# Kernel tuning notes

Hardware: AMD Instinct MI355X
Metric: run time of the kernel (lower is better)

The kernel has to match this reference:

```python
import jax, jax.numpy as jnp
import numpy as np

B, S, H, NH = 8, 1024, 768, 12
DK = H // NH  # 64


def setup_inputs() -> dict:
    key = jax.random.key(0)
    ks = jax.random.split(key, 7)
    sc = 0.02
    return {
        "Q": jax.random.normal(ks[0], (B, S, H), jnp.float32),
        "K": jax.random.normal(ks[1], (B, S, H), jnp.float32),
        "V": jax.random.normal(ks[2], (B, S, H), jnp.float32),
        "Wq": jax.random.normal(ks[3], (H, H), jnp.float32) * sc,
        "Wk": jax.random.normal(ks[4], (H, H), jnp.float32) * sc,
        "Wv": jax.random.normal(ks[5], (H, H), jnp.float32) * sc,
        "Wo": jax.random.normal(ks[6], (H, H), jnp.float32) * sc,
    }


def reference(Q, K, V, Wq, Wk, Wv, Wo):
    # torch Linear(bias=False): y = x @ W.T, weight shape [out, in]
    q = jnp.einsum('bsh,oh->bso', Q, Wq).reshape(B, S, NH, DK)
    k = jnp.einsum('bsh,oh->bso', K, Wk).reshape(B, S, NH, DK)
    v = jnp.einsum('bsh,oh->bso', V, Wv).reshape(B, S, NH, DK)
    # naive SDPA per head: full [B,NH,S,S] score matrix, scale by sqrt(dk)
    scores = jnp.einsum('bqnd,bknd->bnqk', q, k) / jnp.sqrt(jnp.float32(DK))
    w = jax.nn.softmax(scores, axis=-1)
    c = jnp.einsum('bnqk,bknd->bqnd', w, v).reshape(B, S, H)
    return jnp.einsum('bsh,oh->bso', c, Wo)
```

## Files before the change

kernel.cpp:

```cpp
#include <hip/hip_runtime.h>
#include <hip/hip_bf16.h>

#define B_   8
#define S_   1024
#define H_   768
#define NH_  12
#define DK_  64
#define M_   (B_ * S_)

typedef __attribute__((ext_vector_type(8))) short          short8;
typedef __attribute__((ext_vector_type(8))) unsigned short ushort8;
typedef __attribute__((ext_vector_type(4))) unsigned short ushort4v;
typedef __attribute__((ext_vector_type(4))) float          f32x4;

__device__ __forceinline__ unsigned short f2bf(float x) {
    union { __hip_bfloat16 h; unsigned short u; } r;
    r.h = __float2bfloat16(x);
    return r.u;
}

__device__ __forceinline__ unsigned cvtpk_bf16(float lo, float hi) {
    unsigned r;
    asm("v_cvt_pk_bf16_f32 %0, %1, %2" : "=v"(r) : "v"(lo), "v"(hi));
    return r;
}

__global__ __launch_bounds__(256)
void cvt_w(const float* __restrict__ w0, const float* __restrict__ w1,
           const float* __restrict__ w2, const float* __restrict__ w3,
           unsigned short* __restrict__ o0, unsigned short* __restrict__ o1,
           unsigned short* __restrict__ o2, unsigned short* __restrict__ o3)
{
    const int wsel = blockIdx.y;
    const float* src = (wsel == 0) ? w0 : (wsel == 1) ? w1 : (wsel == 2) ? w2 : w3;
    unsigned short* dst = (wsel == 0) ? o0 : (wsel == 1) ? o1 : (wsel == 2) ? o2 : o3;
    const float s = (wsel == 0) ? 0.125f * 1.44269504089f : 1.0f;
    const int i = blockIdx.x * 256 + threadIdx.x;
    const float4 x = ((const float4*)src)[i];
    ushort4v o;
    o[0] = f2bf(x.x * s); o[1] = f2bf(x.y * s);
    o[2] = f2bf(x.z * s); o[3] = f2bf(x.w * s);
    ((ushort4v*)dst)[i] = o;
}

template<bool A_BF16, bool OUT_BF16>
__global__ __launch_bounds__(256)
void gemm_bt(const void* __restrict__ A0, const void* __restrict__ A1,
             const void* __restrict__ A2,
             const unsigned short* __restrict__ W0,
             const unsigned short* __restrict__ W1,
             const unsigned short* __restrict__ W2,
             void* __restrict__ C0, void* __restrict__ C1, void* __restrict__ C2)
{
    __shared__ unsigned short As[128 * 32];
    __shared__ unsigned short Bs[128 * 32];

    const int tid  = threadIdx.x;
    const int z    = blockIdx.z;
    const int bm   = blockIdx.x, bn = blockIdx.y;
    const int w    = tid >> 6, lane = tid & 63;
    const int lg   = lane >> 4, lc = lane & 15;
    const int wm   = (w >> 1) * 64, wn = (w & 1) * 64;

    const void* Av = (z == 0) ? A0 : (z == 1) ? A1 : A2;
    const unsigned short* Bw = (z == 0) ? W0 : (z == 1) ? W1 : W2;
    void* Cv = (z == 0) ? C0 : (z == 1) ? C1 : C2;

    const float*          Af = (const float*)Av;
    const unsigned short* Ah = (const unsigned short*)Av;

    f32x4 acc[4][4] = {};

    for (int k0 = 0; k0 < H_; k0 += 32) {
        if (A_BF16) {
#pragma unroll
            for (int i = 0; i < 2; i++) {
                const int gI = i * 256 + tid;
                const int row = gI >> 2, c8 = (gI & 3) * 8;
                *(ushort8*)&As[row * 32 + c8] =
                    *(const ushort8*)&Ah[(size_t)(bm * 128 + row) * H_ + k0 + c8];
            }
        } else {
#pragma unroll
            for (int i = 0; i < 4; i++) {
                const int gI = i * 256 + tid;
                const int row = gI >> 3, c4 = (gI & 7) * 4;
                const float4 x = *(const float4*)&Af[(size_t)(bm * 128 + row) * H_ + k0 + c4];
                ushort4v o4;
                o4[0] = f2bf(x.x); o4[1] = f2bf(x.y);
                o4[2] = f2bf(x.z); o4[3] = f2bf(x.w);
                *(ushort4v*)&As[row * 32 + c4] = o4;
            }
        }
#pragma unroll
        for (int i = 0; i < 2; i++) {
            const int gI = i * 256 + tid;
            const int row = gI >> 2, c8 = (gI & 3) * 8;
            *(ushort8*)&Bs[row * 32 + c8] =
                *(const ushort8*)&Bw[(size_t)(bn * 128 + row) * H_ + k0 + c8];
        }
        __syncthreads();

        short8 af[4], bfr[4];
#pragma unroll
        for (int mi = 0; mi < 4; mi++)
            af[mi] = *(const short8*)&As[(wm + mi * 16 + lc) * 32 + lg * 8];
#pragma unroll
        for (int ni = 0; ni < 4; ni++)
            bfr[ni] = *(const short8*)&Bs[(wn + ni * 16 + lc) * 32 + lg * 8];
#pragma unroll
        for (int mi = 0; mi < 4; mi++)
#pragma unroll
            for (int ni = 0; ni < 4; ni++)
                acc[mi][ni] = __builtin_amdgcn_mfma_f32_16x16x32_bf16(
                    af[mi], bfr[ni], acc[mi][ni], 0, 0, 0);
        __syncthreads();
    }

#pragma unroll
    for (int mi = 0; mi < 4; mi++)
#pragma unroll
        for (int ni = 0; ni < 4; ni++)
#pragma unroll
            for (int reg = 0; reg < 4; reg++) {
                const int row = bm * 128 + wm + mi * 16 + lg * 4 + reg;
                const int col = bn * 128 + wn + ni * 16 + lc;
                if (OUT_BF16)
                    ((unsigned short*)Cv)[(size_t)row * H_ + col] = f2bf(acc[mi][ni][reg]);
                else
                    ((float*)Cv)[(size_t)row * H_ + col] = acc[mi][ni][reg];
            }
}

__global__ __launch_bounds__(256)
void attn(const unsigned short* __restrict__ q,
          const unsigned short* __restrict__ k,
          const unsigned short* __restrict__ v,
          unsigned short* __restrict__ c)
{
    __shared__ unsigned short Ks[64][72];
    __shared__ unsigned short Vt[64][72];

    const int tid  = threadIdx.x;
    const int qt   = blockIdx.x, h = blockIdx.y, b = blockIdx.z;
    const int wid  = tid >> 6;
    const int lane = tid & 63;
    const int lg   = lane >> 4, lc = lane & 15;
    const int r    = tid >> 2;
    const int d0   = (tid & 3) * 16;
    const int g    = tid & 3;
    const size_t base = (size_t)b * S_ * H_ + (size_t)h * DK_;

    short8 aq[2][2];
#pragma unroll
    for (int m = 0; m < 2; m++)
#pragma unroll
        for (int ks = 0; ks < 2; ks++)
            aq[m][ks] = *(const short8*)
                &q[base + (size_t)(qt * 128 + wid * 32 + m * 16 + lc) * H_ + ks * 32 + lg * 8];

    f32x4 o[2][4] = {};
    float mrow[2] = {-1e30f, -1e30f}, lrow[2] = {0.f, 0.f};

    for (int kt = 0; kt < S_ / 64; kt++) {
        {
            const unsigned short* ksrc = &k[base + (size_t)(kt * 64 + r) * H_ + d0];
            *(ushort8*)&Ks[r][d0]     = *(const ushort8*)ksrc;
            *(ushort8*)&Ks[r][d0 + 8] = *(const ushort8*)(ksrc + 8);
            const unsigned short* vsrc = &v[base + (size_t)(kt * 64 + r) * H_ + d0];
            const ushort8 v0 = *(const ushort8*)vsrc;
            const ushort8 v1 = *(const ushort8*)(vsrc + 8);
            const int colv = r ^ (g << 4);
#pragma unroll
            for (int j = 0; j < 8; j++) Vt[d0 + j][colv]     = v0[j];
#pragma unroll
            for (int j = 0; j < 8; j++) Vt[d0 + 8 + j][colv] = v1[j];
        }
        __syncthreads();

        f32x4 st[2][4] = {};
#pragma unroll
        for (int ni = 0; ni < 4; ni++)
#pragma unroll
            for (int ks = 0; ks < 2; ks++) {
                const short8 bk = *(const short8*)&Ks[ni * 16 + lc][ks * 32 + lg * 8];
                st[0][ni] = __builtin_amdgcn_mfma_f32_16x16x32_bf16(bk, aq[0][ks], st[0][ni], 0, 0, 0);
                st[1][ni] = __builtin_amdgcn_mfma_f32_16x16x32_bf16(bk, aq[1][ks], st[1][ni], 0, 0, 0);
            }

        unsigned pw[2][4][2];
#pragma unroll
        for (int m = 0; m < 2; m++) {
            float pm = st[m][0][0];
#pragma unroll
            for (int ni = 0; ni < 4; ni++)
#pragma unroll
                for (int reg = 0; reg < 4; reg++)
                    pm = fmaxf(pm, st[m][ni][reg]);
            pm = fmaxf(pm, __shfl_xor(pm, 16, 64));
            pm = fmaxf(pm, __shfl_xor(pm, 32, 64));
            const float mnew  = fmaxf(mrow[m], pm);
            const float scale = exp2f(mrow[m] - mnew);
            float psum = 0.f;
#pragma unroll
            for (int ni = 0; ni < 4; ni++)
#pragma unroll
                for (int reg = 0; reg < 4; reg++) {
                    const float p = exp2f(st[m][ni][reg] - mnew);
                    st[m][ni][reg] = p; psum += p;
                }
            psum += __shfl_xor(psum, 16, 64);
            psum += __shfl_xor(psum, 32, 64);
            lrow[m] = lrow[m] * scale + psum;
            mrow[m] = mnew;

            float scr[4];
#pragma unroll
            for (int reg = 0; reg < 4; reg++)
                scr[reg] = __shfl(scale, lg * 4 + reg, 64);
#pragma unroll
            for (int ni = 0; ni < 4; ni++)
#pragma unroll
                for (int reg = 0; reg < 4; reg++)
                    o[m][ni][reg] *= scr[reg];

#pragma unroll
            for (int ni = 0; ni < 4; ni++) {
                pw[m][ni][0] = cvtpk_bf16(st[m][ni][0], st[m][ni][1]);
                pw[m][ni][1] = cvtpk_bf16(st[m][ni][2], st[m][ni][3]);
            }
        }

        const int sl0 = lc + ((lg & 1) << 5);
        const int sl1 = sl0 + 16;
        const bool hi = (lg >> 1) != 0;
        short8 pa[2][2];
#pragma unroll
        for (int m = 0; m < 2; m++)
#pragma unroll
            for (int ks = 0; ks < 2; ks++) {
                const unsigned lo0 = pw[m][2 * ks][0],     lo1 = pw[m][2 * ks][1];
                const unsigned hi0 = pw[m][2 * ks + 1][0], hi1 = pw[m][2 * ks + 1][1];
                union { unsigned u[4]; short8 s8; } pk;
                const unsigned a0l = __shfl(lo0, sl0, 64), a0h = __shfl(hi0, sl0, 64);
                const unsigned a1l = __shfl(lo1, sl0, 64), a1h = __shfl(hi1, sl0, 64);
                const unsigned a2l = __shfl(lo0, sl1, 64), a2h = __shfl(hi0, sl1, 64);
                const unsigned a3l = __shfl(lo1, sl1, 64), a3h = __shfl(hi1, sl1, 64);
                pk.u[0] = hi ? a0h : a0l;
                pk.u[1] = hi ? a1h : a1l;
                pk.u[2] = hi ? a2h : a2l;
                pk.u[3] = hi ? a3h : a3l;
                pa[m][ks] = pk.s8;
            }

#pragma unroll
        for (int ni = 0; ni < 4; ni++)
#pragma unroll
            for (int ks = 0; ks < 2; ks++) {
                const short8 bv = *(const short8*)
                    &Vt[ni * 16 + lc][(ks * 32 + lg * 8) ^ (ni << 4)];
                o[0][ni] = __builtin_amdgcn_mfma_f32_16x16x32_bf16(pa[0][ks], bv, o[0][ni], 0, 0, 0);
                o[1][ni] = __builtin_amdgcn_mfma_f32_16x16x32_bf16(pa[1][ks], bv, o[1][ni], 0, 0, 0);
            }
        __syncthreads();
    }

#pragma unroll
    for (int m = 0; m < 2; m++) {
        const float iv = 1.0f / lrow[m];
#pragma unroll
        for (int reg = 0; reg < 4; reg++) {
            const float ivr = __shfl(iv, lg * 4 + reg, 64);
            const int row = qt * 128 + wid * 32 + m * 16 + lg * 4 + reg;
#pragma unroll
            for (int ni = 0; ni < 4; ni++)
                c[base + (size_t)row * H_ + ni * 16 + lc] = f2bf(o[m][ni][reg] * ivr);
        }
    }
}

extern "C" void kernel_launch(void* const* d_in, const int* in_sizes, int n_in,
                              void* d_out, int out_size, void* d_ws, size_t ws_size,
                              hipStream_t stream)
{
    const float* Q  = (const float*)d_in[0];
    const float* K  = (const float*)d_in[1];
    const float* V  = (const float*)d_in[2];
    const float* Wq = (const float*)d_in[3];
    const float* Wk = (const float*)d_in[4];
    const float* Wv = (const float*)d_in[5];
    const float* Wo = (const float*)d_in[6];

    unsigned short* qb = (unsigned short*)d_ws;
    unsigned short* kb = qb + (size_t)M_ * H_;
    unsigned short* vb = kb + (size_t)M_ * H_;
    unsigned short* cb = vb + (size_t)M_ * H_;
    unsigned short* wq = cb + (size_t)M_ * H_;
    unsigned short* wk = wq + (size_t)H_ * H_;
    unsigned short* wv = wk + (size_t)H_ * H_;
    unsigned short* wo = wv + (size_t)H_ * H_;

    cvt_w<<<dim3(H_ * H_ / 4 / 256, 4), 256, 0, stream>>>(
        Wq, Wk, Wv, Wo, wq, wk, wv, wo);

    gemm_bt<false, true><<<dim3(M_ / 128, H_ / 128, 3), 256, 0, stream>>>(
        Q, K, V, wq, wk, wv, qb, kb, vb);

    attn<<<dim3(S_ / 128, NH_, B_), 256, 0, stream>>>(qb, kb, vb, cb);

    gemm_bt<true, false><<<dim3(M_ / 128, H_ / 128, 1), 256, 0, stream>>>(
        cb, cb, cb, wo, wo, wo, d_out, d_out, d_out);
}
```

Measured before the change: 155.3 us.

## Double-buffer K/V tiles in attention and skip rescale when max is stable

The attention kernel now prefetches the next K/V tile into registers while computing on the current one, and writes it to a second LDS buffer, so there is one barrier per iteration instead of two. It also adds a lazy online-softmax rescale that only updates the running max and rescales the accumulator when the new max exceeds the old by more than 8 (in log2 units). MFMA sections are wrapped with s_setprio to favour matrix issue. This costs extra LDS and registers, which may reduce occupancy. The lazy rescale lets exponentials exceed 1, up to about 2^8, before a rescale.

```diff
diff --git a/kernel.cpp b/kernel.cpp
--- a/kernel.cpp
+++ b/kernel.cpp
@@ -138,8 +138,8 @@
           const unsigned short* __restrict__ v,
           unsigned short* __restrict__ c)
 {
-    __shared__ unsigned short Ks[64][72];
-    __shared__ unsigned short Vt[64][72];
+    __shared__ unsigned short Ks[2][64][72];
+    __shared__ unsigned short Vt[2][64][72];
 
     const int tid  = threadIdx.x;
     const int qt   = blockIdx.x, h = blockIdx.y, b = blockIdx.z;
@@ -150,6 +150,7 @@
     const int d0   = (tid & 3) * 16;
     const int g    = tid & 3;
     const size_t base = (size_t)b * S_ * H_ + (size_t)h * DK_;
+    const int colv = r ^ (g << 4);
 
     short8 aq[2][2];
 #pragma unroll
@@ -162,33 +163,47 @@
     f32x4 o[2][4] = {};
     float mrow[2] = {-1e30f, -1e30f}, lrow[2] = {0.f, 0.f};
 
-    for (int kt = 0; kt < S_ / 64; kt++) {
-        {
-            const unsigned short* ksrc = &k[base + (size_t)(kt * 64 + r) * H_ + d0];
-            *(ushort8*)&Ks[r][d0]     = *(const ushort8*)ksrc;
-            *(ushort8*)&Ks[r][d0 + 8] = *(const ushort8*)(ksrc + 8);
-            const unsigned short* vsrc = &v[base + (size_t)(kt * 64 + r) * H_ + d0];
-            const ushort8 v0 = *(const ushort8*)vsrc;
-            const ushort8 v1 = *(const ushort8*)(vsrc + 8);
-            const int colv = r ^ (g << 4);
-#pragma unroll
-            for (int j = 0; j < 8; j++) Vt[d0 + j][colv]     = v0[j];
-#pragma unroll
-            for (int j = 0; j < 8; j++) Vt[d0 + 8 + j][colv] = v1[j];
-        }
-        __syncthreads();
+    const int NT = S_ / 64;
+
+    ushort8 kr0, kr1, vr0, vr1;
+    {
+        const unsigned short* ksrc = &k[base + (size_t)r * H_ + d0];
+        const unsigned short* vsrc = &v[base + (size_t)r * H_ + d0];
+        kr0 = *(const ushort8*)ksrc; kr1 = *(const ushort8*)(ksrc + 8);
+        vr0 = *(const ushort8*)vsrc; vr1 = *(const ushort8*)(vsrc + 8);
+    }
+    *(ushort8*)&Ks[0][r][d0]     = kr0;
+    *(ushort8*)&Ks[0][r][d0 + 8] = kr1;
+#pragma unroll
+    for (int j = 0; j < 8; j++) Vt[0][d0 + j][colv]     = vr0[j];
+#pragma unroll
+    for (int j = 0; j < 8; j++) Vt[0][d0 + 8 + j][colv] = vr1[j];
+    __syncthreads();
+
+    int cur = 0;
+    for (int kt = 0; kt < NT; kt++) {
+        const bool more = (kt + 1 < NT);
+        if (more) {
+            const unsigned short* ksrc = &k[base + (size_t)((kt + 1) * 64 + r) * H_ + d0];
+            const unsigned short* vsrc = &v[base + (size_t)((kt + 1) * 64 + r) * H_ + d0];
+            kr0 = *(const ushort8*)ksrc; kr1 = *(const ushort8*)(ksrc + 8);
+            vr0 = *(const ushort8*)vsrc; vr1 = *(const ushort8*)(vsrc + 8);
+        }
 
         f32x4 st[2][4] = {};
+        __builtin_amdgcn_s_setprio(1);
 #pragma unroll
         for (int ni = 0; ni < 4; ni++)
 #pragma unroll
             for (int ks = 0; ks < 2; ks++) {
-                const short8 bk = *(const short8*)&Ks[ni * 16 + lc][ks * 32 + lg * 8];
+                const short8 bk = *(const short8*)&Ks[cur][ni * 16 + lc][ks * 32 + lg * 8];
                 st[0][ni] = __builtin_amdgcn_mfma_f32_16x16x32_bf16(bk, aq[0][ks], st[0][ni], 0, 0, 0);
                 st[1][ni] = __builtin_amdgcn_mfma_f32_16x16x32_bf16(bk, aq[1][ks], st[1][ni], 0, 0, 0);
             }
+        __builtin_amdgcn_s_setprio(0);
 
         unsigned pw[2][4][2];
+        float pmax[2];
 #pragma unroll
         for (int m = 0; m < 2; m++) {
             float pm = st[m][0][0];
@@ -199,31 +214,41 @@
                     pm = fmaxf(pm, st[m][ni][reg]);
             pm = fmaxf(pm, __shfl_xor(pm, 16, 64));
             pm = fmaxf(pm, __shfl_xor(pm, 32, 64));
-            const float mnew  = fmaxf(mrow[m], pm);
-            const float scale = exp2f(mrow[m] - mnew);
+            pmax[m] = pm;
+        }
+
+        if (__any((pmax[0] > mrow[0] + 8.f) | (pmax[1] > mrow[1] + 8.f))) {
+#pragma unroll
+            for (int m = 0; m < 2; m++) {
+                const float mnew  = fmaxf(mrow[m], pmax[m]);
+                const float scale = exp2f(mrow[m] - mnew);
+                lrow[m] *= scale;
+                mrow[m]  = mnew;
+                float scr[4];
+#pragma unroll
+                for (int reg = 0; reg < 4; reg++)
+                    scr[reg] = __shfl(scale, lg * 4 + reg, 64);
+#pragma unroll
+                for (int ni = 0; ni < 4; ni++)
+#pragma unroll
+                    for (int reg = 0; reg < 4; reg++)
+                        o[m][ni][reg] *= scr[reg];
+            }
+        }
+
+#pragma unroll
+        for (int m = 0; m < 2; m++) {
             float psum = 0.f;
 #pragma unroll
             for (int ni = 0; ni < 4; ni++)
 #pragma unroll
                 for (int reg = 0; reg < 4; reg++) {
-                    const float p = exp2f(st[m][ni][reg] - mnew);
+                    const float p = exp2f(st[m][ni][reg] - mrow[m]);
                     st[m][ni][reg] = p; psum += p;
                 }
             psum += __shfl_xor(psum, 16, 64);
             psum += __shfl_xor(psum, 32, 64);
-            lrow[m] = lrow[m] * scale + psum;
-            mrow[m] = mnew;
-
-            float scr[4];
-#pragma unroll
-            for (int reg = 0; reg < 4; reg++)
-                scr[reg] = __shfl(scale, lg * 4 + reg, 64);
-#pragma unroll
-            for (int ni = 0; ni < 4; ni++)
-#pragma unroll
-                for (int reg = 0; reg < 4; reg++)
-                    o[m][ni][reg] *= scr[reg];
-
+            lrow[m] += psum;
 #pragma unroll
             for (int ni = 0; ni < 4; ni++) {
                 pw[m][ni][0] = cvtpk_bf16(st[m][ni][0], st[m][ni][1]);
@@ -253,16 +278,28 @@
                 pa[m][ks] = pk.s8;
             }
 
+        __builtin_amdgcn_s_setprio(1);
 #pragma unroll
         for (int ni = 0; ni < 4; ni++)
 #pragma unroll
             for (int ks = 0; ks < 2; ks++) {
                 const short8 bv = *(const short8*)
-                    &Vt[ni * 16 + lc][(ks * 32 + lg * 8) ^ (ni << 4)];
+                    &Vt[cur][ni * 16 + lc][(ks * 32 + lg * 8) ^ (ni << 4)];
                 o[0][ni] = __builtin_amdgcn_mfma_f32_16x16x32_bf16(pa[0][ks], bv, o[0][ni], 0, 0, 0);
                 o[1][ni] = __builtin_amdgcn_mfma_f32_16x16x32_bf16(pa[1][ks], bv, o[1][ni], 0, 0, 0);
             }
+        __builtin_amdgcn_s_setprio(0);
+
+        if (more) {
+            *(ushort8*)&Ks[cur ^ 1][r][d0]     = kr0;
+            *(ushort8*)&Ks[cur ^ 1][r][d0 + 8] = kr1;
+#pragma unroll
+            for (int j = 0; j < 8; j++) Vt[cur ^ 1][d0 + j][colv]     = vr0[j];
+#pragma unroll
+            for (int j = 0; j < 8; j++) Vt[cur ^ 1][d0 + 8 + j][colv] = vr1[j];
+        }
         __syncthreads();
+        cur ^= 1;
     }
 
 #pragma unroll
```

After: 150.7 us. -3.0%, faster.
